# Kernel optimization log

Measured on AMD Instinct MI355X. Metric: run time of the kernel, lower is better.

## Reference

```python
import jax, jax.numpy as jnp
import numpy as np

N_HEAD, D_HEAD, TAU = 16, 64, 1.0

def layer_norm(x, w, b, eps=1e-5):
    mu = jnp.mean(x, axis=-1, keepdims=True)
    var = jnp.var(x, axis=-1, keepdims=True)
    return (x - mu) * jax.lax.rsqrt(var + eps) * w + b

def rel_shift(x):
    # Transformer-XL pad/reshape/slice relative shift on [qlen, klen, bsz, n_head]
    q, k, b, n = x.shape
    xp = jnp.concatenate([jnp.zeros((q, 1, b, n), x.dtype), x], axis=1)
    xp = xp.reshape(k + 1, q, b, n)
    return xp[1:].reshape(q, k, b, n)

def gru_gate(x, y, Wr, Ur, Wz, bz, Uz, Wg, Ug):
    z = jax.nn.sigmoid(y @ Wz + bz + x @ Uz)
    r = jax.nn.sigmoid(y @ Wr + x @ Ur)
    h = jnp.tanh(y @ Wg + (r * x) @ Ug)
    return (1.0 - z) * x + z * h

def setup_inputs():
    key = jax.random.key(0)
    ks = iter(jax.random.split(key, 40))
    qlen, mlen, bsz, d_model, d_inner = 512, 512, 4, 1024, 4096
    klen = qlen + mlen
    s = 0.02
    p = {}
    p['w'] = jax.random.normal(next(ks), (qlen, bsz, d_model), jnp.float32)
    p['mems'] = jax.random.normal(next(ks), (mlen, bsz, d_model), jnp.float32)
    p['r'] = jax.random.normal(next(ks), (klen, d_model), jnp.float32)
    p['r_w_bias'] = jax.random.normal(next(ks), (N_HEAD, D_HEAD), jnp.float32) * s
    p['r_r_bias'] = jax.random.normal(next(ks), (N_HEAD, D_HEAD), jnp.float32) * s
    i = jnp.arange(qlen)[:, None]; j = jnp.arange(klen)[None, :]
    p['attn_mask'] = (j > i + mlen)[:, :, None]  # causal-with-memory [qlen, klen, 1]
    p['ln_a_w'] = jnp.ones((d_model,), jnp.float32); p['ln_a_b'] = jnp.zeros((d_model,), jnp.float32)
    p['W_qkv'] = jax.random.normal(next(ks), (d_model, 3 * N_HEAD * D_HEAD), jnp.float32) * s
    p['W_r'] = jax.random.normal(next(ks), (d_model, N_HEAD * D_HEAD), jnp.float32) * s
    p['W_o'] = jax.random.normal(next(ks), (N_HEAD * D_HEAD, d_model), jnp.float32) * s
    p['ln2_w'] = jnp.ones((d_model,), jnp.float32); p['ln2_b'] = jnp.zeros((d_model,), jnp.float32)
    p['ff_W1'] = jax.random.normal(next(ks), (d_model, d_inner), jnp.float32) * s
    p['ff_b1'] = jnp.zeros((d_inner,), jnp.float32)
    p['ff_W2'] = jax.random.normal(next(ks), (d_inner, d_model), jnp.float32) * s
    p['ff_b2'] = jnp.zeros((d_model,), jnp.float32)
    for g in ('gm', 'gp'):
        for nm in ('Wr', 'Ur', 'Uz', 'Wg', 'Ug', 'Wz'):
            p[f'{g}_{nm}'] = jax.random.normal(next(ks), (d_model, d_model), jnp.float32) * s
        p[f'{g}_bz'] = jnp.full((d_model,), -2.0, jnp.float32)  # GRUGate init_bias
    return p

def _forward(w, mems, r, r_w_bias, r_r_bias, attn_mask, ln_a_w, ln_a_b, W_qkv, W_r, W_o,
             ln2_w, ln2_b, ff_W1, ff_b1, ff_W2, ff_b2,
             gm_Wr, gm_Ur, gm_Wz, gm_bz, gm_Uz, gm_Wg, gm_Ug,
             gp_Wr, gp_Ur, gp_Wz, gp_bz, gp_Uz, gp_Wg, gp_Ug):
    qlen, bsz, d_model = w.shape
    cat = jnp.concatenate([mems, w], axis=0)          # [klen, b, d]
    klen = cat.shape[0]
    # stable version: pre-LN inside attention sublayer
    heads = layer_norm(cat, ln_a_w, ln_a_b) @ W_qkv    # [klen, b, 3*n*d]
    q, k, v = jnp.split(heads, 3, axis=-1)
    q = q[-qlen:].reshape(qlen, bsz, N_HEAD, D_HEAD)
    k = k.reshape(klen, bsz, N_HEAD, D_HEAD)
    v = v.reshape(klen, bsz, N_HEAD, D_HEAD)
    r_k = (r @ W_r).reshape(klen, N_HEAD, D_HEAD)      # [rlen, n, d]
    AC = jnp.einsum('ibnd,jbnd->ijbn', q + r_w_bias, k)
    BD = rel_shift(jnp.einsum('ibnd,jnd->ijbn', q + r_r_bias, r_k))
    score = (AC + BD) * (1.0 / D_HEAD ** 0.5)
    mask = attn_mask[:, :, :, None]                    # [q, k, 1or b, 1]
    score = jnp.where(mask, -jnp.inf, score)
    prob = jax.nn.softmax(score * TAU, axis=1)
    p = jax.lax.stop_gradient(prob)
    safe = jnp.where(p > 0, p, 1.0)
    ent = jnp.where(mask, 0.0, -p * jnp.log(safe))
    attn_entropy = ent.sum(axis=1).mean(axis=(0, 1))   # [n_head]
    attn_out = jnp.einsum('ijbn,jbnd->ibnd', prob, v).reshape(qlen, bsz, N_HEAD * D_HEAD) @ W_o
    # GRU-gated residual around attention (with ReLU, GTrXL-style stable version)
    o1 = gru_gate(w, jax.nn.relu(attn_out), gm_Wr, gm_Ur, gm_Wz, gm_bz, gm_Uz, gm_Wg, gm_Ug)
    ff = jax.nn.relu(layer_norm(o1, ln2_w, ln2_b) @ ff_W1 + ff_b1) @ ff_W2 + ff_b2
    out = gru_gate(o1, jax.nn.relu(ff), gp_Wr, gp_Ur, gp_Wz, gp_bz, gp_Uz, gp_Wg, gp_Ug)
    return out, attn_entropy

def reference(w, mems, r, r_w_bias, r_r_bias, attn_mask, ln_a_w, ln_a_b, W_qkv, W_r, W_o,
              ln2_w, ln2_b, ff_W1, ff_b1, ff_W2, ff_b2,
              gm_Wr, gm_Ur, gm_Wz, gm_bz, gm_Uz, gm_Wg, gm_Ug,
              gp_Wr, gp_Ur, gp_Wz, gp_bz, gp_Uz, gp_Wg, gp_Ug):
    return _forward(w, mems, r, r_w_bias, r_r_bias, attn_mask, ln_a_w, ln_a_b, W_qkv, W_r, W_o,
                    ln2_w, ln2_b, ff_W1, ff_b1, ff_W2, ff_b2,
                    gm_Wr, gm_Ur, gm_Wz, gm_bz, gm_Uz, gm_Wg, gm_Ug,
                    gp_Wr, gp_Ur, gp_Wz, gp_bz, gp_Uz, gp_Wg, gp_Ug)
```

## Files before the change

kernel.cpp:

```cpp
#include <hip/hip_runtime.h>
#include <math.h>


#define QLEN 512
#define MLEN 512
#define KLEN 1024
#define BSZ  4
#define DM   1024
#define DI   4096
#define NH   16
#define DH   64
#define HC   (3*DM)
#define HR   (KLEN*BSZ)
#define NROWS (QLEN*BSZ)

enum { ACT_NONE = 0, ACT_RELU = 1, ACT_SIG = 2, ACT_TANH = 3 };
enum { MODE_NORM = 0, MODE_QKV = 1, MODE_RK = 2 };

using short8 = __attribute__((ext_vector_type(8))) short;
using f32x4  = __attribute__((ext_vector_type(4))) float;

__device__ __forceinline__ unsigned short f2bf(float f) {
  union { float f; unsigned u; } v;
  v.f = f;
  unsigned r = v.u + 0x7FFFu + ((v.u >> 16) & 1u);
  return (unsigned short)(r >> 16);
}
__device__ __forceinline__ float bf2f(unsigned short u) {
  union { unsigned u; float f; } v;
  v.u = ((unsigned)u) << 16;
  return v.f;
}

__device__ __forceinline__ void async16(const void* g, void* l) {
  __builtin_amdgcn_global_load_lds(
      (const __attribute__((address_space(1))) void*)g,
      (__attribute__((address_space(3))) void*)l, 16, 0, 0);
}

__device__ __forceinline__ float waveSum(float v) {
#pragma unroll
  for (int o = 32; o; o >>= 1) v += __shfl_down(v, o, 64);
  return v;
}

template <bool CONCAT>
__global__ __launch_bounds__(256) void ln_kernel(
    const float* __restrict__ a, const float* __restrict__ a2,
    const float* __restrict__ wt, const float* __restrict__ bs,
    unsigned short* __restrict__ dst) {
  const int row = blockIdx.x;
  const int tid = threadIdx.x;
  const float* srow;
  if (CONCAT)
    srow = (row < MLEN * BSZ) ? a + (size_t)row * DM
                              : a2 + (size_t)(row - MLEN * BSZ) * DM;
  else
    srow = a + (size_t)row * DM;
  float4 x = *(const float4*)(srow + tid * 4);
  float s = x.x + x.y + x.z + x.w;
  float q = x.x * x.x + x.y * x.y + x.z * x.z + x.w * x.w;
  __shared__ float2 red[4];
  float2 p;
  p.x = waveSum(s);
  p.y = waveSum(q);
  if ((tid & 63) == 0) red[tid >> 6] = p;
  __syncthreads();
  float S = red[0].x + red[1].x + red[2].x + red[3].x;
  float Q = red[0].y + red[1].y + red[2].y + red[3].y;
  const float inv = 1.0f / DM;
  float mu = S * inv;
  float var = Q * inv - mu * mu;
  float rs = rsqrtf(var + 1e-5f);
  float4 w4 = *(const float4*)(wt + tid * 4);
  float4 b4 = *(const float4*)(bs + tid * 4);
  ushort4 o = {f2bf((x.x - mu) * rs * w4.x + b4.x),
               f2bf((x.y - mu) * rs * w4.y + b4.y),
               f2bf((x.z - mu) * rs * w4.z + b4.z),
               f2bf((x.w - mu) * rs * w4.w + b4.w)};
  *(ushort4*)(dst + (size_t)row * DM + tid * 4) = o;
}

template <int BM, int BN, int ACT, bool BIAS, int MODE, bool OUT16>
__global__ __launch_bounds__(256) void mgemm(
    const unsigned short* __restrict__ A, const unsigned short* __restrict__ Bt,
    void* __restrict__ Cv, const float* __restrict__ bias,
    const float* __restrict__ xsrc,
    unsigned short* __restrict__ g0, unsigned short* __restrict__ g1,
    unsigned short* __restrict__ g2,
    int M, int N, int K, int ldc) {
  (void)M; (void)N;
  constexpr int TM = (BM == 128) ? 4 : 1;
  constexpr int TN = (BM == 128) ? 4 : BN / 16;
  constexpr int ACH = BM / 32;
  constexpr int BCH = BN / 32;
  __shared__ __align__(16) unsigned short As[2][BM][64];
  __shared__ __align__(16) unsigned short Bs[2][BN][64];
  const int tid = threadIdx.x;
  const int wave = tid >> 6, lane = tid & 63;
  const int row0 = blockIdx.y * BM, col0 = blockIdx.x * BN;
  const int wm = (BM == 128) ? (wave >> 1) * 64 : wave * 16;
  const int wn = (BM == 128) ? (wave & 1) * 64 : 0;
  const int lr = lane & 15, quad = lane >> 4;
  const int l7 = lr & 7;

  const int sr = lane >> 3, sc16 = lane & 7;
  const int scol = (sc16 ^ sr) * 8;

  const unsigned short* gA[ACH];
  const unsigned short* gB[BCH];
#pragma unroll
  for (int c = 0; c < ACH; c++)
    gA[c] = A + (size_t)(row0 + c * 32 + wave * 8 + sr) * K + scol;
#pragma unroll
  for (int c = 0; c < BCH; c++)
    gB[c] = Bt + (size_t)(col0 + c * 32 + wave * 8 + sr) * K + scol;

  f32x4 acc[TM][TN];
#pragma unroll
  for (int a = 0; a < TM; a++)
#pragma unroll
    for (int b = 0; b < TN; b++) {
      acc[a][b][0] = 0.f; acc[a][b][1] = 0.f;
      acc[a][b][2] = 0.f; acc[a][b][3] = 0.f;
    }

#pragma unroll
  for (int c = 0; c < ACH; c++) {
    async16(gA[c], &As[0][c * 32 + wave * 8][0]);
    gA[c] += 64;
  }
#pragma unroll
  for (int c = 0; c < BCH; c++) {
    async16(gB[c], &Bs[0][c * 32 + wave * 8][0]);
    gB[c] += 64;
  }
  __syncthreads();

  const int nt = K >> 6;
  int cur = 0;
  for (int t = 0; t < nt; ++t) {
    if (t + 1 < nt) {
      const int nx = cur ^ 1;
#pragma unroll
      for (int c = 0; c < ACH; c++) {
        async16(gA[c], &As[nx][c * 32 + wave * 8][0]);
        gA[c] += 64;
      }
#pragma unroll
      for (int c = 0; c < BCH; c++) {
        async16(gB[c], &Bs[nx][c * 32 + wave * 8][0]);
        gB[c] += 64;
      }
      __builtin_amdgcn_sched_barrier(0);
    }
#pragma unroll
    for (int ks = 0; ks < 2; ks++) {
      const int cs = ((ks * 4 + quad) ^ l7) * 8;
      short8 af[TM], bfr[TN];
#pragma unroll
      for (int mi = 0; mi < TM; mi++)
        af[mi] = *(const short8*)&As[cur][wm + mi * 16 + lr][cs];
#pragma unroll
      for (int ni = 0; ni < TN; ni++)
        bfr[ni] = *(const short8*)&Bs[cur][wn + ni * 16 + lr][cs];
      __builtin_amdgcn_s_setprio(1);
#pragma unroll
      for (int mi = 0; mi < TM; mi++)
#pragma unroll
        for (int ni = 0; ni < TN; ni++)
          acc[mi][ni] = __builtin_amdgcn_mfma_f32_16x16x32_bf16(
              af[mi], bfr[ni], acc[mi][ni], 0, 0, 0);
      __builtin_amdgcn_s_setprio(0);
    }
    __syncthreads();
    cur ^= 1;
  }

  const int cbase = col0 + wn + lr;
  float bv[TN];
  if constexpr (BIAS) {
#pragma unroll
    for (int ni = 0; ni < TN; ni++) bv[ni] = bias[cbase + ni * 16];
  }
  const int region = (MODE == MODE_QKV) ? (col0 >> 10) : 0;
#pragma unroll
  for (int mi = 0; mi < TM; mi++) {
    const int r0 = row0 + wm + mi * 16 + quad * 4;
#pragma unroll
    for (int ni = 0; ni < TN; ni++) {
      const int cc = cbase + ni * 16;
#pragma unroll
      for (int e = 0; e < 4; e++) {
        float v = acc[mi][ni][e];
        if constexpr (BIAS) v += bv[ni];
        if constexpr (ACT == ACT_RELU) v = fmaxf(v, 0.f);
        else if constexpr (ACT == ACT_SIG) v = 1.f / (1.f + expf(-v));
        else if constexpr (ACT == ACT_TANH) v = tanhf(v);
        if constexpr (MODE == MODE_QKV) {
          const int rr = r0 + e;
          const int pos = rr >> 2, bb = rr & 3;
          const int cl = cc & 1023, hn = cl >> 6, d = cl & 63;
          const unsigned short hv = f2bf(v);
          if (region == 0) {
            if (pos >= MLEN)
              g0[(((size_t)(bb * NH + hn) * QLEN + (pos - MLEN)) << 6) + d] = hv;
          } else if (region == 1) {
            g1[(((size_t)(bb * NH + hn) * KLEN + pos) << 6) + d] = hv;
          } else {
            g2[(((size_t)(bb * NH + hn) * DH + d) << 10) + pos] = hv;
          }
        } else if constexpr (MODE == MODE_RK) {
          const int hn = cc >> 6, d = cc & 63;
          g0[(((size_t)hn * KLEN + (r0 + e)) << 6) + d] = f2bf(v);
        } else {
          if constexpr (OUT16)
            ((unsigned short*)Cv)[(size_t)(r0 + e) * ldc + cc] = f2bf(v);
          else
            ((float*)Cv)[(size_t)(r0 + e) * ldc + cc] = v;
        }
      }
      if (xsrc) {
#pragma unroll
        for (int e = 0; e < 4; e++)
          ((unsigned short*)Cv)[(size_t)(r0 + e) * ldc + 1024 + cc] =
              f2bf(xsrc[(size_t)(r0 + e) * 1024 + cc]);
      }
    }
  }
}

#define FA_PAD 72
#define PT_PAD 76
__global__ __launch_bounds__(256) void fused_attn(
    const unsigned short* __restrict__ Q_g,
    const unsigned short* __restrict__ K_g,
    const unsigned short* __restrict__ V_gT,
    const unsigned short* __restrict__ rk_g,
    const float* __restrict__ rwb, const float* __restrict__ rrb,
    unsigned short* __restrict__ attnb,
    float* __restrict__ ent) {
  const int nb = blockIdx.x;
  const int n = nb & 15, b = nb >> 4;
  const int it0 = blockIdx.y;
  const int i0 = it0 * 64;
  const int tid = threadIdx.x;
  const int wave = tid >> 6, lane = tid & 63;
  const int lr = lane & 15, quad = lane >> 4;
  const int wm = wave * 16;

  __shared__ __align__(16) unsigned short Ks[64][FA_PAD];
  __shared__ __align__(16) unsigned short Vt[64][FA_PAD];
  __shared__ __align__(16) unsigned short Rk[64][FA_PAD];
  __shared__ __align__(16) unsigned short BDr[4][2][16][PT_PAD];
  __shared__ __align__(16) unsigned short Pt[4][16][PT_PAD];

  const unsigned short* Qb = Q_g + (((size_t)(b * NH + n) * QLEN + i0) << 6);
  const unsigned short* Kb = K_g + (((size_t)(b * NH + n) * KLEN) << 6);
  const unsigned short* Vb = V_gT + (((size_t)(b * NH + n) * DH) << 10);
  const unsigned short* Rb = rk_g + (((size_t)n * KLEN) << 6);

  const int row0 = tid >> 3, vc = (tid & 7) * 8;

  short8 kr0 = *(const short8*)(Kb + (size_t)row0 * 64 + vc);
  short8 kr1 = *(const short8*)(Kb + (size_t)(row0 + 32) * 64 + vc);
  short8 vr0 = *(const short8*)(Vb + (size_t)row0 * 1024 + vc);
  short8 vr1 = *(const short8*)(Vb + (size_t)(row0 + 32) * 1024 + vc);
  short8 rr0, rr1;
  {
    const unsigned short* Rt = Rb + ((size_t)(7 - it0) << 12);
    rr0 = *(const short8*)(Rt + (size_t)row0 * 64 + vc);
    rr1 = *(const short8*)(Rt + (size_t)(row0 + 32) * 64 + vc);
  }
  __builtin_amdgcn_sched_barrier(0);

  short8 aw[2], ar[2];
#pragma unroll
  for (int ks = 0; ks < 2; ks++) {
    const int d0 = ks * 32 + quad * 8;
    short8 qv = *(const short8*)(Qb + (wm + lr) * 64 + d0);
#pragma unroll
    for (int e = 0; e < 8; e++) {
      float f = bf2f((unsigned short)qv[e]);
      aw[ks][e] = (short)f2bf((f + rwb[n * DH + d0 + e]) * 0.125f);
      ar[ks][e] = (short)f2bf((f + rrb[n * DH + d0 + e]) * 0.125f);
    }
  }

  *(short8*)&Ks[row0][vc] = kr0;
  *(short8*)&Ks[row0 + 32][vc] = kr1;
  *(short8*)&Vt[row0][vc] = vr0;
  *(short8*)&Vt[row0 + 32][vc] = vr1;
  *(short8*)&Rk[row0][vc] = rr0;
  *(short8*)&Rk[row0 + 32][vc] = rr1;
  __syncthreads();

  {
    const unsigned short* Rt = Rb + ((size_t)(8 - it0) << 12);
    rr0 = *(const short8*)(Rt + (size_t)row0 * 64 + vc);
    rr1 = *(const short8*)(Rt + (size_t)(row0 + 32) * 64 + vc);
  }
  __builtin_amdgcn_sched_barrier(0);
  {
    f32x4 bd[4];
#pragma unroll
    for (int ni = 0; ni < 4; ni++) {
      bd[ni][0] = 0.f; bd[ni][1] = 0.f; bd[ni][2] = 0.f; bd[ni][3] = 0.f;
    }
    __builtin_amdgcn_s_setprio(1);
#pragma unroll
    for (int ks = 0; ks < 2; ks++)
#pragma unroll
      for (int ni = 0; ni < 4; ni++) {
        short8 br = *(const short8*)&Rk[ni * 16 + lr][ks * 32 + quad * 8];
        bd[ni] = __builtin_amdgcn_mfma_f32_16x16x32_bf16(ar[ks], br, bd[ni], 0, 0, 0);
      }
    __builtin_amdgcn_s_setprio(0);
#pragma unroll
    for (int ni = 0; ni < 4; ni++)
#pragma unroll
      for (int e = 0; e < 4; e++)
        BDr[wave][0][quad * 4 + e][ni * 16 + lr] = f2bf(bd[ni][e]);
  }
  __syncthreads();
  *(short8*)&Rk[row0][vc] = rr0;
  *(short8*)&Rk[row0 + 32][vc] = rr1;
  __syncthreads();

  f32x4 O[4];
#pragma unroll
  for (int d = 0; d < 4; d++) {
    O[d][0] = 0.f; O[d][1] = 0.f; O[d][2] = 0.f; O[d][3] = 0.f;
  }
  float mrow[4] = {-INFINITY, -INFINITY, -INFINITY, -INFINITY};
  float lrow[4] = {0.f, 0.f, 0.f, 0.f};
  float erow[4] = {0.f, 0.f, 0.f, 0.f};

  const int nj = it0 + 9;
  for (int t = 0; t < nj; t++) {
    const int j0 = t * 64;
    const int rtile = 8 - it0 + t;
    const int hi = (t + 1) & 1, lo = t & 1;
    const bool pfK = (t + 1 < nj);
    const bool pfR = pfK && (rtile + 1 < 16);

    if (pfK) {
      kr0 = *(const short8*)(Kb + (size_t)(j0 + 64 + row0) * 64 + vc);
      kr1 = *(const short8*)(Kb + (size_t)(j0 + 96 + row0) * 64 + vc);
      vr0 = *(const short8*)(Vb + (size_t)row0 * 1024 + j0 + 64 + vc);
      vr1 = *(const short8*)(Vb + (size_t)(row0 + 32) * 1024 + j0 + 64 + vc);
    }
    if (pfR) {
      const unsigned short* Rt = Rb + ((size_t)(rtile + 1) << 12);
      rr0 = *(const short8*)(Rt + (size_t)row0 * 64 + vc);
      rr1 = *(const short8*)(Rt + (size_t)(row0 + 32) * 64 + vc);
    }
    __builtin_amdgcn_sched_barrier(0);

    f32x4 ac[4], bd[4];
#pragma unroll
    for (int ni = 0; ni < 4; ni++) {
      ac[ni][0] = 0.f; ac[ni][1] = 0.f; ac[ni][2] = 0.f; ac[ni][3] = 0.f;
      bd[ni][0] = 0.f; bd[ni][1] = 0.f; bd[ni][2] = 0.f; bd[ni][3] = 0.f;
    }
    __builtin_amdgcn_s_setprio(1);
#pragma unroll
    for (int ks = 0; ks < 2; ks++)
#pragma unroll
      for (int ni = 0; ni < 4; ni++) {
        short8 bk = *(const short8*)&Ks[ni * 16 + lr][ks * 32 + quad * 8];
        ac[ni] = __builtin_amdgcn_mfma_f32_16x16x32_bf16(aw[ks], bk, ac[ni], 0, 0, 0);
      }
    if (rtile < 16) {
#pragma unroll
      for (int ks = 0; ks < 2; ks++)
#pragma unroll
        for (int ni = 0; ni < 4; ni++) {
          short8 br = *(const short8*)&Rk[ni * 16 + lr][ks * 32 + quad * 8];
          bd[ni] = __builtin_amdgcn_mfma_f32_16x16x32_bf16(ar[ks], br, bd[ni], 0, 0, 0);
        }
    }
    __builtin_amdgcn_s_setprio(0);
    if (rtile < 16) {
#pragma unroll
      for (int ni = 0; ni < 4; ni++)
#pragma unroll
        for (int e = 0; e < 4; e++)
          BDr[wave][hi][quad * 4 + e][ni * 16 + lr] = f2bf(bd[ni][e]);
    }

    float sc[4][4];
#pragma unroll
    for (int ni = 0; ni < 4; ni++) {
      const int jl = ni * 16 + lr;
#pragma unroll
      for (int e = 0; e < 4; e++) {
        const int il = wm + quad * 4 + e;
        const int jjrel = jl + 63 - il;
        const float bdv =
            bf2f(BDr[wave][jjrel >= 64 ? hi : lo][quad * 4 + e][jjrel & 63]);
        const bool masked = (j0 + jl) > (i0 + il + MLEN);
        sc[ni][e] = masked ? -INFINITY : (ac[ni][e] + bdv);
      }
    }
#pragma unroll
    for (int e = 0; e < 4; e++) {
      float tm = fmaxf(fmaxf(sc[0][e], sc[1][e]), fmaxf(sc[2][e], sc[3][e]));
#pragma unroll
      for (int msk = 1; msk < 16; msk <<= 1)
        tm = fmaxf(tm, __shfl_xor(tm, msk, 64));
      const float mo = mrow[e];
      const float mn = fmaxf(mo, tm);
      const float al = __expf(mo - mn);
      float psum = 0.f, pes = 0.f, ps[4];
#pragma unroll
      for (int ni = 0; ni < 4; ni++) {
        const float s_ = sc[ni][e];
        const float p = __expf(s_ - mn);
        ps[ni] = p;
        psum += p;
        pes += (p > 0.f) ? p * s_ : 0.f;
      }
      lrow[e] = lrow[e] * al + psum;
      erow[e] = erow[e] * al + pes;
      mrow[e] = mn;
#pragma unroll
      for (int d = 0; d < 4; d++) O[d][e] *= al;
#pragma unroll
      for (int ni = 0; ni < 4; ni++)
        Pt[wave][quad * 4 + e][ni * 16 + lr] = f2bf(ps[ni]);
    }
    __builtin_amdgcn_s_setprio(1);
#pragma unroll
    for (int ks = 0; ks < 2; ks++) {
      short8 ap = *(const short8*)&Pt[wave][lr][ks * 32 + quad * 8];
#pragma unroll
      for (int d = 0; d < 4; d++) {
        short8 bv = *(const short8*)&Vt[d * 16 + lr][ks * 32 + quad * 8];
        O[d] = __builtin_amdgcn_mfma_f32_16x16x32_bf16(ap, bv, O[d], 0, 0, 0);
      }
    }
    __builtin_amdgcn_s_setprio(0);

    if (pfK) {
      __syncthreads();
      *(short8*)&Ks[row0][vc] = kr0;
      *(short8*)&Ks[row0 + 32][vc] = kr1;
      *(short8*)&Vt[row0][vc] = vr0;
      *(short8*)&Vt[row0 + 32][vc] = vr1;
      if (pfR) {
        *(short8*)&Rk[row0][vc] = rr0;
        *(short8*)&Rk[row0 + 32][vc] = rr1;
      }
      __syncthreads();
    }
  }

#pragma unroll
  for (int e = 0; e < 4; e++) {
#pragma unroll
    for (int msk = 1; msk < 16; msk <<= 1) {
      lrow[e] += __shfl_xor(lrow[e], msk, 64);
      erow[e] += __shfl_xor(erow[e], msk, 64);
    }
  }
#pragma unroll
  for (int e = 0; e < 4; e++) {
    const int il = wm + quad * 4 + e;
    const float invl = 1.f / lrow[e];
#pragma unroll
    for (int d = 0; d < 4; d++)
      attnb[((size_t)(i0 + il) * BSZ + b) * DM + n * DH + d * 16 + lr] =
          f2bf(O[d][e] * invl);
  }
  float esum = 0.f;
#pragma unroll
  for (int e = 0; e < 4; e++)
    esum += mrow[e] + __logf(lrow[e]) - erow[e] / lrow[e];
  esum += __shfl_xor(esum, 16, 64);
  esum += __shfl_xor(esum, 32, 64);
  if (lane == 0) atomicAdd(ent + n, esum * (1.f / (QLEN * BSZ)));
}

#define MAXD 18
struct TDesc {
  const float* src;
  unsigned short* dst;
  int N, dstStride, colOff, tilesX, tileBase;
};
struct TDescs { TDesc d[MAXD]; int n; };

__global__ __launch_bounds__(256) void castT_batch(TDescs ds) {
  const int bid = blockIdx.x;
  int di = 0;
  while (di + 1 < ds.n && ds.d[di + 1].tileBase <= bid) di++;
  const TDesc t = ds.d[di];
  const int lt = bid - t.tileBase;
  const int n0 = (lt % t.tilesX) * 64, k0 = (lt / t.tilesX) * 64;
  __shared__ float T[64][65];
  const int tid = threadIdx.x;
  const int tx = tid & 15, ty = tid >> 4;
#pragma unroll
  for (int l = 0; l < 4; l++) {
    const int k = ty + l * 16;
    float4 v = *(const float4*)(t.src + (size_t)(k0 + k) * t.N + n0 + tx * 4);
    T[tx * 4 + 0][k] = v.x;
    T[tx * 4 + 1][k] = v.y;
    T[tx * 4 + 2][k] = v.z;
    T[tx * 4 + 3][k] = v.w;
  }
  __syncthreads();
#pragma unroll
  for (int l = 0; l < 4; l++) {
    const int n = ty + l * 16;
    ushort4 o = {f2bf(T[n][tx * 4 + 0]), f2bf(T[n][tx * 4 + 1]),
                 f2bf(T[n][tx * 4 + 2]), f2bf(T[n][tx * 4 + 3])};
    *(ushort4*)(t.dst + (size_t)(n0 + n) * t.dstStride + t.colOff + k0 +
                tx * 4) = o;
  }
}

__global__ __launch_bounds__(256) void castRows(
    const float* __restrict__ src, unsigned short* __restrict__ dst,
    int dstStride) {
  const size_t e0 = ((size_t)blockIdx.x * 256 + threadIdx.x) * 4;
  const size_t m = e0 >> 10, c = e0 & 1023;
  float4 v = *(const float4*)(src + e0);
  ushort4 o = {f2bf(v.x), f2bf(v.y), f2bf(v.z), f2bf(v.w)};
  *(ushort4*)(dst + m * dstStride + c) = o;
}

__global__ __launch_bounds__(256) void ew_rx(
    const float* __restrict__ zr, const float* __restrict__ x,
    unsigned short* __restrict__ ayx) {
  const size_t e0 = ((size_t)blockIdx.x * 256 + threadIdx.x) * 4;
  const size_t m = e0 >> 10, c = e0 & 1023;
  float4 rr = *(const float4*)(zr + m * 2048 + 1024 + c);
  float4 xx = *(const float4*)(x + e0);
  ushort4 o = {f2bf(rr.x * xx.x), f2bf(rr.y * xx.y),
               f2bf(rr.z * xx.z), f2bf(rr.w * xx.w)};
  *(ushort4*)(ayx + m * 2048 + 1024 + c) = o;
}
__global__ __launch_bounds__(256) void ew_out(
    const float* __restrict__ zr, const float* __restrict__ x,
    const float* __restrict__ h, float* __restrict__ o) {
  const size_t e0 = ((size_t)blockIdx.x * 256 + threadIdx.x) * 4;
  const size_t m = e0 >> 10, c = e0 & 1023;
  float4 zz = *(const float4*)(zr + m * 2048 + c);
  float4 xx = *(const float4*)(x + e0);
  float4 hh = *(const float4*)(h + e0);
  float4 r;
  r.x = (1.f - zz.x) * xx.x + zz.x * hh.x;
  r.y = (1.f - zz.y) * xx.y + zz.y * hh.y;
  r.z = (1.f - zz.z) * xx.z + zz.z * hh.z;
  r.w = (1.f - zz.w) * xx.w + zz.w * hh.w;
  *(float4*)(o + e0) = r;
}
__global__ __launch_bounds__(256) void ew_out_ln(
    const float* __restrict__ zr, const float* __restrict__ x,
    const float* __restrict__ h, const float* __restrict__ lw,
    const float* __restrict__ lb, float* __restrict__ ofp,
    unsigned short* __restrict__ obf) {
  const int m = blockIdx.x;
  const int tid = threadIdx.x;
  const int c = tid * 4;
  float4 zz = *(const float4*)(zr + (size_t)m * 2048 + c);
  float4 xx = *(const float4*)(x + (size_t)m * 1024 + c);
  float4 hh = *(const float4*)(h + (size_t)m * 1024 + c);
  float ov[4];
  ov[0] = (1.f - zz.x) * xx.x + zz.x * hh.x;
  ov[1] = (1.f - zz.y) * xx.y + zz.y * hh.y;
  ov[2] = (1.f - zz.z) * xx.z + zz.z * hh.z;
  ov[3] = (1.f - zz.w) * xx.w + zz.w * hh.w;
  *(float4*)(ofp + (size_t)m * 1024 + c) = *(float4*)ov;
  float s = ov[0] + ov[1] + ov[2] + ov[3];
  float q = ov[0] * ov[0] + ov[1] * ov[1] + ov[2] * ov[2] + ov[3] * ov[3];
  __shared__ float2 red[4];
  float2 p;
  p.x = waveSum(s);
  p.y = waveSum(q);
  if ((tid & 63) == 0) red[tid >> 6] = p;
  __syncthreads();
  float S = red[0].x + red[1].x + red[2].x + red[3].x;
  float Q = red[0].y + red[1].y + red[2].y + red[3].y;
  const float inv = 1.0f / DM;
  float mu = S * inv;
  float var = Q * inv - mu * mu;
  float rs = rsqrtf(var + 1e-5f);
  float4 w4 = *(const float4*)(lw + c);
  float4 b4 = *(const float4*)(lb + c);
  ushort4 o = {f2bf((ov[0] - mu) * rs * w4.x + b4.x),
               f2bf((ov[1] - mu) * rs * w4.y + b4.y),
               f2bf((ov[2] - mu) * rs * w4.z + b4.z),
               f2bf((ov[3] - mu) * rs * w4.w + b4.w)};
  *(ushort4*)(obf + (size_t)m * 1024 + c) = o;
}

__global__ void misc_init(const float* __restrict__ gmbz,
                          const float* __restrict__ gpbz,
                          float* __restrict__ bias_gm,
                          float* __restrict__ bias_gp,
                          float* __restrict__ ent) {
  const int i = blockIdx.x * 256 + threadIdx.x;
  if (i < 2048) {
    bias_gm[i] = (i < 1024) ? gmbz[i] : 0.f;
    bias_gp[i] = (i < 1024) ? gpbz[i] : 0.f;
  }
  if (i < 16) ent[i] = 0.f;
}

extern "C" void kernel_launch(void* const* d_in, const int* in_sizes, int n_in,
                              void* d_out, int out_size, void* d_ws,
                              size_t ws_size, hipStream_t stream) {
  (void)in_sizes; (void)n_in; (void)out_size; (void)ws_size;
  const float* w      = (const float*)d_in[0];
  const float* r      = (const float*)d_in[2];
  const float* rwb    = (const float*)d_in[3];
  const float* rrb    = (const float*)d_in[4];
  const float* mems   = (const float*)d_in[1];
  const float* ln_a_w = (const float*)d_in[6];
  const float* ln_a_b = (const float*)d_in[7];
  const float* W_qkv  = (const float*)d_in[8];
  const float* W_r    = (const float*)d_in[9];
  const float* W_o    = (const float*)d_in[10];
  const float* ln2_w  = (const float*)d_in[11];
  const float* ln2_b  = (const float*)d_in[12];
  const float* ff_W1  = (const float*)d_in[13];
  const float* ff_b1  = (const float*)d_in[14];
  const float* ff_W2  = (const float*)d_in[15];
  const float* ff_b2  = (const float*)d_in[16];
  const float* gm_Wr  = (const float*)d_in[17];
  const float* gm_Ur  = (const float*)d_in[18];
  const float* gm_Uz  = (const float*)d_in[19];
  const float* gm_Wg  = (const float*)d_in[20];
  const float* gm_Ug  = (const float*)d_in[21];
  const float* gm_Wz  = (const float*)d_in[22];
  const float* gm_bz  = (const float*)d_in[23];
  const float* gp_Wr  = (const float*)d_in[24];
  const float* gp_Ur  = (const float*)d_in[25];
  const float* gp_Uz  = (const float*)d_in[26];
  const float* gp_Wg  = (const float*)d_in[27];
  const float* gp_Ug  = (const float*)d_in[28];
  const float* gp_Wz  = (const float*)d_in[29];
  const float* gp_bz  = (const float*)d_in[30];

  float* out = (float*)d_out;
  float* ent = out + (size_t)NROWS * DM;

  char* base = (char*)d_ws;
  size_t o = 0;
  unsigned short* wt_qkv   = (unsigned short*)(base + o); o += (size_t)3072 * 1024 * 2;
  unsigned short* wt_r     = (unsigned short*)(base + o); o += (size_t)1024 * 1024 * 2;
  unsigned short* wt_o     = (unsigned short*)(base + o); o += (size_t)1024 * 1024 * 2;
  unsigned short* wt_gm_zr = (unsigned short*)(base + o); o += (size_t)2048 * 2048 * 2;
  unsigned short* wt_gm_g  = (unsigned short*)(base + o); o += (size_t)1024 * 2048 * 2;
  unsigned short* wt_gp_zr = (unsigned short*)(base + o); o += (size_t)2048 * 2048 * 2;
  unsigned short* wt_gp_g  = (unsigned short*)(base + o); o += (size_t)1024 * 2048 * 2;
  unsigned short* wt_ff1   = (unsigned short*)(base + o); o += (size_t)4096 * 1024 * 2;
  unsigned short* wt_ff2   = (unsigned short*)(base + o); o += (size_t)1024 * 4096 * 2;
  float* bias_gm = (float*)(base + o); o += 2048 * 4;
  float* bias_gp = (float*)(base + o); o += 2048 * 4;
  unsigned short* Q_g  = (unsigned short*)(base + o); o += (size_t)BSZ * NH * QLEN * DH * 2;
  unsigned short* K_g  = (unsigned short*)(base + o); o += (size_t)BSZ * NH * KLEN * DH * 2;
  unsigned short* V_gT = (unsigned short*)(base + o); o += (size_t)BSZ * NH * DH * KLEN * 2;
  unsigned short* rk_g = (unsigned short*)(base + o); o += (size_t)NH * KLEN * DH * 2;
  unsigned short* lncat_bf = (unsigned short*)(base + o); o += (size_t)HR * DM * 2;
  unsigned short* r_bf = (unsigned short*)(base + o); o += (size_t)KLEN * DM * 2;
  unsigned short* attnb_bf = (unsigned short*)(base + o); o += (size_t)NROWS * DM * 2;
  unsigned short* Ayx = (unsigned short*)(base + o); o += (size_t)NROWS * 2048 * 2;
  float* zr   = (float*)(base + o); o += (size_t)NROWS * 2048 * 4;
  float* hbuf = (float*)(base + o); o += (size_t)NROWS * DM * 4;
  float* o1f  = (float*)(base + o); o += (size_t)NROWS * DM * 4;
  unsigned short* lnb_bf = (unsigned short*)(base + o); o += (size_t)NROWS * DM * 2;
  unsigned short* ffh_bf = (unsigned short*)(base + o); o += (size_t)NROWS * DI * 2;

  TDescs ds;
  int nt = 0, tb = 0;
  auto add = [&](const float* s, unsigned short* d, int N, int K, int stride,
                 int colOff) {
    ds.d[nt] = {s, d, N, stride, colOff, N / 64, tb};
    tb += (N / 64) * (K / 64);
    nt++;
  };
  add(W_qkv, wt_qkv, 3072, 1024, 1024, 0);
  add(W_r, wt_r, 1024, 1024, 1024, 0);
  add(W_o, wt_o, 1024, 1024, 1024, 0);
  add(gm_Wz, wt_gm_zr, 1024, 1024, 2048, 0);
  add(gm_Uz, wt_gm_zr, 1024, 1024, 2048, 1024);
  add(gm_Wr, wt_gm_zr + (size_t)1024 * 2048, 1024, 1024, 2048, 0);
  add(gm_Ur, wt_gm_zr + (size_t)1024 * 2048, 1024, 1024, 2048, 1024);
  add(gm_Wg, wt_gm_g, 1024, 1024, 2048, 0);
  add(gm_Ug, wt_gm_g, 1024, 1024, 2048, 1024);
  add(gp_Wz, wt_gp_zr, 1024, 1024, 2048, 0);
  add(gp_Uz, wt_gp_zr, 1024, 1024, 2048, 1024);
  add(gp_Wr, wt_gp_zr + (size_t)1024 * 2048, 1024, 1024, 2048, 0);
  add(gp_Ur, wt_gp_zr + (size_t)1024 * 2048, 1024, 1024, 2048, 1024);
  add(gp_Wg, wt_gp_g, 1024, 1024, 2048, 0);
  add(gp_Ug, wt_gp_g, 1024, 1024, 2048, 1024);
  add(ff_W1, wt_ff1, 4096, 1024, 1024, 0);
  add(ff_W2, wt_ff2, 1024, 4096, 4096, 0);
  ds.n = nt;
  castT_batch<<<tb, 256, 0, stream>>>(ds);
  misc_init<<<8, 256, 0, stream>>>(gm_bz, gp_bz, bias_gm, bias_gp, ent);

  ln_kernel<true><<<HR, 256, 0, stream>>>(mems, w, ln_a_w, ln_a_b, lncat_bf);
  mgemm<128, 128, ACT_NONE, false, MODE_QKV, true>
      <<<dim3(24, 32), 256, 0, stream>>>(
      lncat_bf, wt_qkv, nullptr, nullptr, nullptr, Q_g, K_g, V_gT,
      HR, HC, 1024, 0);
  castRows<<<1024, 256, 0, stream>>>(r, r_bf, 1024);
  mgemm<64, 64, ACT_NONE, false, MODE_RK, true>
      <<<dim3(16, 16), 256, 0, stream>>>(
      r_bf, wt_r, nullptr, nullptr, nullptr, rk_g, nullptr, nullptr,
      KLEN, 1024, 1024, 0);

  fused_attn<<<dim3(NH * BSZ, 8), 256, 0, stream>>>(Q_g, K_g, V_gT, rk_g,
                                                    rwb, rrb, attnb_bf, ent);

  mgemm<64, 64, ACT_RELU, false, MODE_NORM, true>
      <<<dim3(16, 32), 256, 0, stream>>>(
      attnb_bf, wt_o, Ayx, nullptr, w, nullptr, nullptr, nullptr,
      NROWS, 1024, 1024, 2048);
  mgemm<64, 128, ACT_SIG, true, MODE_NORM, false>
      <<<dim3(16, 32), 256, 0, stream>>>(
      Ayx, wt_gm_zr, zr, bias_gm, nullptr, nullptr, nullptr, nullptr,
      NROWS, 2048, 2048, 2048);
  ew_rx<<<2048, 256, 0, stream>>>(zr, w, Ayx);
  mgemm<64, 64, ACT_TANH, false, MODE_NORM, false>
      <<<dim3(16, 32), 256, 0, stream>>>(
      Ayx, wt_gm_g, hbuf, nullptr, nullptr, nullptr, nullptr, nullptr,
      NROWS, 1024, 2048, 1024);
  ew_out_ln<<<NROWS, 256, 0, stream>>>(zr, w, hbuf, ln2_w, ln2_b, o1f, lnb_bf);

  mgemm<128, 128, ACT_RELU, true, MODE_NORM, true>
      <<<dim3(32, 16), 256, 0, stream>>>(
      lnb_bf, wt_ff1, ffh_bf, ff_b1, nullptr, nullptr, nullptr, nullptr,
      NROWS, DI, 1024, DI);
  mgemm<64, 64, ACT_RELU, true, MODE_NORM, true>
      <<<dim3(16, 32), 256, 0, stream>>>(
      ffh_bf, wt_ff2, Ayx, ff_b2, o1f, nullptr, nullptr, nullptr,
      NROWS, 1024, DI, 2048);

  mgemm<64, 128, ACT_SIG, true, MODE_NORM, false>
      <<<dim3(16, 32), 256, 0, stream>>>(
      Ayx, wt_gp_zr, zr, bias_gp, nullptr, nullptr, nullptr, nullptr,
      NROWS, 2048, 2048, 2048);
  ew_rx<<<2048, 256, 0, stream>>>(zr, o1f, Ayx);
  mgemm<64, 64, ACT_TANH, false, MODE_NORM, false>
      <<<dim3(16, 32), 256, 0, stream>>>(
      Ayx, wt_gp_g, hbuf, nullptr, nullptr, nullptr, nullptr, nullptr,
      NROWS, 1024, 2048, 1024);
  ew_out<<<2048, 256, 0, stream>>>(zr, o1f, hbuf, out);
}
```

Measured before the change: 548.2 us.

## Split-K the GRU and FF2 GEMMs with 128x128 tiles and fused reductions

Adds a blockIdx.z split-K mode to the GEMM kernel with a separate lda, so each z-slice writes fp32 partial sums to its own buffer. The gate GEMMs (K=2048) split 2-way or 4-way and FF2 (K=4096) splits 4-way, all moved to 128x128 tiles. The bias, sigmoid, tanh and ReLU epilogues move into the elementwise kernels that sum the partials. The goal is more blocks in flight for small-N GEMMs with long K and larger tiles, paid for with extra fp32 partial-buffer traffic and wider elementwise reads.

```diff
diff --git a/kernel.cpp b/kernel.cpp
--- a/kernel.cpp
+++ b/kernel.cpp
@@ -88,8 +88,8 @@
     const float* __restrict__ xsrc,
     unsigned short* __restrict__ g0, unsigned short* __restrict__ g1,
     unsigned short* __restrict__ g2,
-    int M, int N, int K, int ldc) {
-  (void)M; (void)N;
+    int M, int N, int K, int ldc, int lda) {
+  (void)N;
   constexpr int TM = (BM == 128) ? 4 : 1;
   constexpr int TN = (BM == 128) ? 4 : BN / 16;
   constexpr int ACH = BM / 32;
@@ -99,6 +99,8 @@
   const int tid = threadIdx.x;
   const int wave = tid >> 6, lane = tid & 63;
   const int row0 = blockIdx.y * BM, col0 = blockIdx.x * BN;
+  const int kz = blockIdx.z;
+  const size_t koff = (size_t)kz * K;
   const int wm = (BM == 128) ? (wave >> 1) * 64 : wave * 16;
   const int wn = (BM == 128) ? (wave & 1) * 64 : 0;
   const int lr = lane & 15, quad = lane >> 4;
@@ -111,10 +113,10 @@
   const unsigned short* gB[BCH];
 #pragma unroll
   for (int c = 0; c < ACH; c++)
-    gA[c] = A + (size_t)(row0 + c * 32 + wave * 8 + sr) * K + scol;
+    gA[c] = A + (size_t)(row0 + c * 32 + wave * 8 + sr) * lda + koff + scol;
 #pragma unroll
   for (int c = 0; c < BCH; c++)
-    gB[c] = Bt + (size_t)(col0 + c * 32 + wave * 8 + sr) * K + scol;
+    gB[c] = Bt + (size_t)(col0 + c * 32 + wave * 8 + sr) * lda + koff + scol;
 
   f32x4 acc[TM][TN];
 #pragma unroll
@@ -183,6 +185,7 @@
 #pragma unroll
     for (int ni = 0; ni < TN; ni++) bv[ni] = bias[cbase + ni * 16];
   }
+  float* Cf = (float*)Cv + (size_t)kz * M * ldc;
   const int region = (MODE == MODE_QKV) ? (col0 >> 10) : 0;
 #pragma unroll
   for (int mi = 0; mi < TM; mi++) {
@@ -217,7 +220,7 @@
           if constexpr (OUT16)
             ((unsigned short*)Cv)[(size_t)(r0 + e) * ldc + cc] = f2bf(v);
           else
-            ((float*)Cv)[(size_t)(r0 + e) * ldc + cc] = v;
+            Cf[(size_t)(r0 + e) * ldc + cc] = v;
         }
       }
       if (xsrc) {
@@ -530,49 +533,96 @@
   *(ushort4*)(dst + m * dstStride + c) = o;
 }
 
-__global__ __launch_bounds__(256) void ew_rx(
-    const float* __restrict__ zr, const float* __restrict__ x,
-    unsigned short* __restrict__ ayx) {
+__device__ __forceinline__ float sigf(float v) { return 1.f / (1.f + expf(-v)); }
+
+__global__ __launch_bounds__(256) void ew_rx2(
+    const float* __restrict__ P0, const float* __restrict__ P1,
+    const float* __restrict__ x, unsigned short* __restrict__ ayx) {
   const size_t e0 = ((size_t)blockIdx.x * 256 + threadIdx.x) * 4;
   const size_t m = e0 >> 10, c = e0 & 1023;
-  float4 rr = *(const float4*)(zr + m * 2048 + 1024 + c);
+  const size_t ri = m * 2048 + 1024 + c;
+  float4 a = *(const float4*)(P0 + ri);
+  float4 b = *(const float4*)(P1 + ri);
   float4 xx = *(const float4*)(x + e0);
-  ushort4 o = {f2bf(rr.x * xx.x), f2bf(rr.y * xx.y),
-               f2bf(rr.z * xx.z), f2bf(rr.w * xx.w)};
-  *(ushort4*)(ayx + m * 2048 + 1024 + c) = o;
-}
-__global__ __launch_bounds__(256) void ew_out(
-    const float* __restrict__ zr, const float* __restrict__ x,
-    const float* __restrict__ h, float* __restrict__ o) {
+  ushort4 o = {f2bf(sigf(a.x + b.x) * xx.x), f2bf(sigf(a.y + b.y) * xx.y),
+               f2bf(sigf(a.z + b.z) * xx.z), f2bf(sigf(a.w + b.w) * xx.w)};
+  *(ushort4*)(ayx + ri) = o;
+}
+
+__global__ __launch_bounds__(256) void ew_out2(
+    const float* __restrict__ P0, const float* __restrict__ P1,
+    const float* __restrict__ bz, const float* __restrict__ x,
+    const float* __restrict__ G, float* __restrict__ o) {
   const size_t e0 = ((size_t)blockIdx.x * 256 + threadIdx.x) * 4;
   const size_t m = e0 >> 10, c = e0 & 1023;
-  float4 zz = *(const float4*)(zr + m * 2048 + c);
+  const size_t zi = m * 2048 + c;
+  const size_t GS = (size_t)NROWS * 1024;
+  float4 a = *(const float4*)(P0 + zi);
+  float4 b = *(const float4*)(P1 + zi);
+  float4 bb = *(const float4*)(bz + c);
+  float4 g0 = *(const float4*)(G + e0);
+  float4 g1 = *(const float4*)(G + GS + e0);
+  float4 g2 = *(const float4*)(G + 2 * GS + e0);
+  float4 g3 = *(const float4*)(G + 3 * GS + e0);
   float4 xx = *(const float4*)(x + e0);
-  float4 hh = *(const float4*)(h + e0);
   float4 r;
-  r.x = (1.f - zz.x) * xx.x + zz.x * hh.x;
-  r.y = (1.f - zz.y) * xx.y + zz.y * hh.y;
-  r.z = (1.f - zz.z) * xx.z + zz.z * hh.z;
-  r.w = (1.f - zz.w) * xx.w + zz.w * hh.w;
+  {
+    float z = sigf(a.x + b.x + bb.x), h = tanhf(g0.x + g1.x + g2.x + g3.x);
+    r.x = (1.f - z) * xx.x + z * h;
+  }
+  {
+    float z = sigf(a.y + b.y + bb.y), h = tanhf(g0.y + g1.y + g2.y + g3.y);
+    r.y = (1.f - z) * xx.y + z * h;
+  }
+  {
+    float z = sigf(a.z + b.z + bb.z), h = tanhf(g0.z + g1.z + g2.z + g3.z);
+    r.z = (1.f - z) * xx.z + z * h;
+  }
+  {
+    float z = sigf(a.w + b.w + bb.w), h = tanhf(g0.w + g1.w + g2.w + g3.w);
+    r.w = (1.f - z) * xx.w + z * h;
+  }
   *(float4*)(o + e0) = r;
 }
-__global__ __launch_bounds__(256) void ew_out_ln(
-    const float* __restrict__ zr, const float* __restrict__ x,
-    const float* __restrict__ h, const float* __restrict__ lw,
+
+__global__ __launch_bounds__(256) void ew_out_ln2(
+    const float* __restrict__ P0, const float* __restrict__ P1,
+    const float* __restrict__ bz, const float* __restrict__ x,
+    const float* __restrict__ G, const float* __restrict__ lw,
     const float* __restrict__ lb, float* __restrict__ ofp,
     unsigned short* __restrict__ obf) {
   const int m = blockIdx.x;
   const int tid = threadIdx.x;
   const int c = tid * 4;
-  float4 zz = *(const float4*)(zr + (size_t)m * 2048 + c);
-  float4 xx = *(const float4*)(x + (size_t)m * 1024 + c);
-  float4 hh = *(const float4*)(h + (size_t)m * 1024 + c);
+  const size_t zi = (size_t)m * 2048 + c;
+  const size_t gi = (size_t)m * 1024 + c;
+  const size_t GS = (size_t)NROWS * 1024;
+  float4 a = *(const float4*)(P0 + zi);
+  float4 b = *(const float4*)(P1 + zi);
+  float4 bb = *(const float4*)(bz + c);
+  float4 g0 = *(const float4*)(G + gi);
+  float4 g1 = *(const float4*)(G + GS + gi);
+  float4 g2 = *(const float4*)(G + 2 * GS + gi);
+  float4 g3 = *(const float4*)(G + 3 * GS + gi);
+  float4 xx = *(const float4*)(x + gi);
   float ov[4];
-  ov[0] = (1.f - zz.x) * xx.x + zz.x * hh.x;
-  ov[1] = (1.f - zz.y) * xx.y + zz.y * hh.y;
-  ov[2] = (1.f - zz.z) * xx.z + zz.z * hh.z;
-  ov[3] = (1.f - zz.w) * xx.w + zz.w * hh.w;
-  *(float4*)(ofp + (size_t)m * 1024 + c) = *(float4*)ov;
+  {
+    float z = sigf(a.x + b.x + bb.x), h = tanhf(g0.x + g1.x + g2.x + g3.x);
+    ov[0] = (1.f - z) * xx.x + z * h;
+  }
+  {
+    float z = sigf(a.y + b.y + bb.y), h = tanhf(g0.y + g1.y + g2.y + g3.y);
+    ov[1] = (1.f - z) * xx.y + z * h;
+  }
+  {
+    float z = sigf(a.z + b.z + bb.z), h = tanhf(g0.z + g1.z + g2.z + g3.z);
+    ov[2] = (1.f - z) * xx.z + z * h;
+  }
+  {
+    float z = sigf(a.w + b.w + bb.w), h = tanhf(g0.w + g1.w + g2.w + g3.w);
+    ov[3] = (1.f - z) * xx.w + z * h;
+  }
+  *(float4*)(ofp + gi) = *(float4*)ov;
   float s = ov[0] + ov[1] + ov[2] + ov[3];
   float q = ov[0] * ov[0] + ov[1] * ov[1] + ov[2] * ov[2] + ov[3] * ov[3];
   __shared__ float2 red[4];
@@ -596,16 +646,29 @@
   *(ushort4*)(obf + (size_t)m * 1024 + c) = o;
 }
 
-__global__ void misc_init(const float* __restrict__ gmbz,
-                          const float* __restrict__ gpbz,
-                          float* __restrict__ bias_gm,
-                          float* __restrict__ bias_gp,
-                          float* __restrict__ ent) {
-  const int i = blockIdx.x * 256 + threadIdx.x;
-  if (i < 2048) {
-    bias_gm[i] = (i < 1024) ? gmbz[i] : 0.f;
-    bias_gp[i] = (i < 1024) ? gpbz[i] : 0.f;
-  }
+__global__ __launch_bounds__(256) void red_ff2(
+    const float* __restrict__ G, const float* __restrict__ bias,
+    const float* __restrict__ o1f, unsigned short* __restrict__ ayx) {
+  const size_t e0 = ((size_t)blockIdx.x * 256 + threadIdx.x) * 4;
+  const size_t m = e0 >> 10, c = e0 & 1023;
+  const size_t GS = (size_t)NROWS * 1024;
+  float4 g0 = *(const float4*)(G + e0);
+  float4 g1 = *(const float4*)(G + GS + e0);
+  float4 g2 = *(const float4*)(G + 2 * GS + e0);
+  float4 g3 = *(const float4*)(G + 3 * GS + e0);
+  float4 bb = *(const float4*)(bias + c);
+  float4 xx = *(const float4*)(o1f + e0);
+  ushort4 o = {f2bf(fmaxf(g0.x + g1.x + g2.x + g3.x + bb.x, 0.f)),
+               f2bf(fmaxf(g0.y + g1.y + g2.y + g3.y + bb.y, 0.f)),
+               f2bf(fmaxf(g0.z + g1.z + g2.z + g3.z + bb.z, 0.f)),
+               f2bf(fmaxf(g0.w + g1.w + g2.w + g3.w + bb.w, 0.f))};
+  *(ushort4*)(ayx + m * 2048 + c) = o;
+  ushort4 ox = {f2bf(xx.x), f2bf(xx.y), f2bf(xx.z), f2bf(xx.w)};
+  *(ushort4*)(ayx + m * 2048 + 1024 + c) = ox;
+}
+
+__global__ void ent_init(float* __restrict__ ent) {
+  const int i = threadIdx.x;
   if (i < 16) ent[i] = 0.f;
 }
 
@@ -658,8 +721,6 @@
   unsigned short* wt_gp_g  = (unsigned short*)(base + o); o += (size_t)1024 * 2048 * 2;
   unsigned short* wt_ff1   = (unsigned short*)(base + o); o += (size_t)4096 * 1024 * 2;
   unsigned short* wt_ff2   = (unsigned short*)(base + o); o += (size_t)1024 * 4096 * 2;
-  float* bias_gm = (float*)(base + o); o += 2048 * 4;
-  float* bias_gp = (float*)(base + o); o += 2048 * 4;
   unsigned short* Q_g  = (unsigned short*)(base + o); o += (size_t)BSZ * NH * QLEN * DH * 2;
   unsigned short* K_g  = (unsigned short*)(base + o); o += (size_t)BSZ * NH * KLEN * DH * 2;
   unsigned short* V_gT = (unsigned short*)(base + o); o += (size_t)BSZ * NH * DH * KLEN * 2;
@@ -668,11 +729,12 @@
   unsigned short* r_bf = (unsigned short*)(base + o); o += (size_t)KLEN * DM * 2;
   unsigned short* attnb_bf = (unsigned short*)(base + o); o += (size_t)NROWS * DM * 2;
   unsigned short* Ayx = (unsigned short*)(base + o); o += (size_t)NROWS * 2048 * 2;
-  float* zr   = (float*)(base + o); o += (size_t)NROWS * 2048 * 4;
-  float* hbuf = (float*)(base + o); o += (size_t)NROWS * DM * 4;
+  float* zrP  = (float*)(base + o); o += (size_t)2 * NROWS * 2048 * 4;
+  float* gP   = (float*)(base + o); o += (size_t)4 * NROWS * 1024 * 4;
   float* o1f  = (float*)(base + o); o += (size_t)NROWS * DM * 4;
   unsigned short* lnb_bf = (unsigned short*)(base + o); o += (size_t)NROWS * DM * 2;
   unsigned short* ffh_bf = (unsigned short*)(base + o); o += (size_t)NROWS * DI * 2;
+  float* zrP1 = zrP + (size_t)NROWS * 2048;
 
   TDescs ds;
   int nt = 0, tb = 0;
@@ -701,18 +763,18 @@
   add(ff_W2, wt_ff2, 1024, 4096, 4096, 0);
   ds.n = nt;
   castT_batch<<<tb, 256, 0, stream>>>(ds);
-  misc_init<<<8, 256, 0, stream>>>(gm_bz, gp_bz, bias_gm, bias_gp, ent);
+  ent_init<<<1, 64, 0, stream>>>(ent);
 
   ln_kernel<true><<<HR, 256, 0, stream>>>(mems, w, ln_a_w, ln_a_b, lncat_bf);
   mgemm<128, 128, ACT_NONE, false, MODE_QKV, true>
       <<<dim3(24, 32), 256, 0, stream>>>(
       lncat_bf, wt_qkv, nullptr, nullptr, nullptr, Q_g, K_g, V_gT,
-      HR, HC, 1024, 0);
+      HR, HC, 1024, 0, 1024);
   castRows<<<1024, 256, 0, stream>>>(r, r_bf, 1024);
   mgemm<64, 64, ACT_NONE, false, MODE_RK, true>
       <<<dim3(16, 16), 256, 0, stream>>>(
       r_bf, wt_r, nullptr, nullptr, nullptr, rk_g, nullptr, nullptr,
-      KLEN, 1024, 1024, 0);
+      KLEN, 1024, 1024, 0, 1024);
 
   fused_attn<<<dim3(NH * BSZ, 8), 256, 0, stream>>>(Q_g, K_g, V_gT, rk_g,
                                                     rwb, rrb, attnb_bf, ent);
@@ -720,35 +782,37 @@
   mgemm<64, 64, ACT_RELU, false, MODE_NORM, true>
       <<<dim3(16, 32), 256, 0, stream>>>(
       attnb_bf, wt_o, Ayx, nullptr, w, nullptr, nullptr, nullptr,
-      NROWS, 1024, 1024, 2048);
-  mgemm<64, 128, ACT_SIG, true, MODE_NORM, false>
-      <<<dim3(16, 32), 256, 0, stream>>>(
-      Ayx, wt_gm_zr, zr, bias_gm, nullptr, nullptr, nullptr, nullptr,
-      NROWS, 2048, 2048, 2048);
-  ew_rx<<<2048, 256, 0, stream>>>(zr, w, Ayx);
-  mgemm<64, 64, ACT_TANH, false, MODE_NORM, false>
-      <<<dim3(16, 32), 256, 0, stream>>>(
-      Ayx, wt_gm_g, hbuf, nullptr, nullptr, nullptr, nullptr, nullptr,
-      NROWS, 1024, 2048, 1024);
-  ew_out_ln<<<NROWS, 256, 0, stream>>>(zr, w, hbuf, ln2_w, ln2_b, o1f, lnb_bf);
+      NROWS, 1024, 1024, 2048, 1024);
+  mgemm<128, 128, ACT_NONE, false, MODE_NORM, false>
+      <<<dim3(16, 16, 2), 256, 0, stream>>>(
+      Ayx, wt_gm_zr, zrP, nullptr, nullptr, nullptr, nullptr, nullptr,
+      NROWS, 2048, 1024, 2048, 2048);
+  ew_rx2<<<2048, 256, 0, stream>>>(zrP, zrP1, w, Ayx);
+  mgemm<128, 128, ACT_NONE, false, MODE_NORM, false>
+      <<<dim3(8, 16, 4), 256, 0, stream>>>(
+      Ayx, wt_gm_g, gP, nullptr, nullptr, nullptr, nullptr, nullptr,
+      NROWS, 1024, 512, 1024, 2048);
+  ew_out_ln2<<<NROWS, 256, 0, stream>>>(zrP, zrP1, gm_bz, w, gP,
+                                        ln2_w, ln2_b, o1f, lnb_bf);
 
   mgemm<128, 128, ACT_RELU, true, MODE_NORM, true>
       <<<dim3(32, 16), 256, 0, stream>>>(
       lnb_bf, wt_ff1, ffh_bf, ff_b1, nullptr, nullptr, nullptr, nullptr,
-      NROWS, DI, 1024, DI);
-  mgemm<64, 64, ACT_RELU, true, MODE_NORM, true>
-      <<<dim3(16, 32), 256, 0, stream>>>(
-      ffh_bf, wt_ff2, Ayx, ff_b2, o1f, nullptr, nullptr, nullptr,
-      NROWS, 1024, DI, 2048);
-
-  mgemm<64, 128, ACT_SIG, true, MODE_NORM, false>
-      <<<dim3(16, 32), 256, 0, stream>>>(
-      Ayx, wt_gp_zr, zr, bias_gp, nullptr, nullptr, nullptr, nullptr,
-      NROWS, 2048, 2048, 2048);
-  ew_rx<<<2048, 256, 0, stream>>>(zr, o1f, Ayx);
-  mgemm<64, 64, ACT_TANH, false, MODE_NORM, false>
-      <<<dim3(16, 32), 256, 0, stream>>>(
-      Ayx, wt_gp_g, hbuf, nullptr, nullptr, nullptr, nullptr, nullptr,
-      NROWS, 1024, 2048, 1024);
-  ew_out<<<2048, 256, 0, stream>>>(zr, o1f, hbuf, out);
-}
+      NROWS, DI, 1024, DI, 1024);
+  mgemm<128, 128, ACT_NONE, false, MODE_NORM, false>
+      <<<dim3(8, 16, 4), 256, 0, stream>>>(
+      ffh_bf, wt_ff2, gP, nullptr, nullptr, nullptr, nullptr, nullptr,
+      NROWS, 1024, 1024, 1024, 4096);
+  red_ff2<<<2048, 256, 0, stream>>>(gP, ff_b2, o1f, Ayx);
+
+  mgemm<128, 128, ACT_NONE, false, MODE_NORM, false>
+      <<<dim3(16, 16, 2), 256, 0, stream>>>(
+      Ayx, wt_gp_zr, zrP, nullptr, nullptr, nullptr, nullptr, nullptr,
+      NROWS, 2048, 1024, 2048, 2048);
+  ew_rx2<<<2048, 256, 0, stream>>>(zrP, zrP1, o1f, Ayx);
+  mgemm<128, 128, ACT_NONE, false, MODE_NORM, false>
+      <<<dim3(8, 16, 4), 256, 0, stream>>>(
+      Ayx, wt_gp_g, gP, nullptr, nullptr, nullptr, nullptr, nullptr,
+      NROWS, 1024, 512, 1024, 2048);
+  ew_out2<<<2048, 256, 0, stream>>>(zrP, zrP1, gp_bz, o1f, gP, out);
+}
```

Result: faster. 525.5 us (-4.1%).
